# Kernel tuning notes

Measured on AMD Instinct MI355X. Metric: run time of the kernel, lower is better.

## Reference

```python
import jax, jax.numpy as jnp
import numpy as np


def _laplacian(A):
    # D^{-1/2} A D^{-1/2}; original builds diag matrices and does D@A@D,
    # which is mathematically identical to broadcast row/col scaling.
    d = jnp.sum(A, axis=-1)
    dinv = 1.0 / jnp.sqrt(d)
    return A * dinv[:, None] * dinv[None, :]


def _poly(A, theta):
    # P = I + sum_{i=1..k} theta_sig[i-1] * A^i  (theta passed through sigmoid)
    t = jax.nn.sigmoid(theta)
    N = A.shape[-1]
    P = jnp.eye(N, dtype=A.dtype)
    seg = P
    for i in range(theta.shape[0]):  # k is small (2), static loop over poly order
        seg = seg @ A
        P = P + seg * t[i]
    return P


def setup_inputs() -> dict:
    key = jax.random.key(0)
    k1, k2, k3, k4 = jax.random.split(key, 4)
    N, DIN, DOUT, K_CHEB = 4096, 64, 64, 2
    return {
        "x": jax.random.normal(k1, (N, DIN), dtype=jnp.float32),
        "A": jax.random.uniform(k2, (N, N), dtype=jnp.float32),  # positive row sums
        "theta": jax.random.normal(k3, (K_CHEB,), dtype=jnp.float32),
        "W": jax.random.normal(k4, (DOUT, DIN), dtype=jnp.float32) / np.float32(np.sqrt(DIN)),
        "b": jnp.zeros((DOUT,), dtype=jnp.float32),
        "k": 4,
    }


def reference(x, A, theta, W, b, k):
    S = _laplacian(A)
    S = _poly(S, theta)
    S = _laplacian(S)
    # double argsort over last dim = per-row descending rank of each entry
    rank = jnp.argsort(jnp.argsort(-S, axis=-1), axis=-1)
    mask = jnp.where(rank < k, jnp.float32(1.0), jnp.float32(0.0))
    S = S * mask  # keep only top-k entries per row
    x = S @ x     # [N,N] @ [N,DIN]
    return x @ W.T + b  # nn.Linear
```

## Files before the change

### kernel.cpp

```cpp
#include <hip/hip_runtime.h>
#include <hip/hip_bf16.h>
#include <float.h>
#include <math.h>

#define N 4096
#define DIN 64

typedef signed char i8_t;
typedef signed char i8x4 __attribute__((ext_vector_type(4)));
typedef int i32x4 __attribute__((ext_vector_type(4)));
typedef float f32x4 __attribute__((ext_vector_type(4)));

__device__ __forceinline__ void gload16(const void* g, void* l) {
    __builtin_amdgcn_global_load_lds((const __attribute__((address_space(1))) void*)g,
                                     (__attribute__((address_space(3))) void*)l,
                                     16, 0, 0);
}

__device__ __forceinline__ float block_reduce_sum(float s) {
    __shared__ float red[4];
    #pragma unroll
    for (int off = 32; off; off >>= 1) s += __shfl_down(s, off);
    if ((threadIdx.x & 63) == 0) red[threadIdx.x >> 6] = s;
    __syncthreads();
    return red[0] + red[1] + red[2] + red[3];
}

__device__ __forceinline__ bool better(float v1, int j1, float v2, int j2) {
    return v1 > v2 || (v1 == v2 && j1 < j2);
}
__device__ __forceinline__ void ins4(float v, int j, float bv[4], int bj[4]) {
    if (!better(v, j, bv[3], bj[3])) return;
    bv[3] = v; bj[3] = j;
    if (better(bv[3], bj[3], bv[2], bj[2])) {
        float tv = bv[2]; int tj = bj[2]; bv[2] = bv[3]; bj[2] = bj[3]; bv[3] = tv; bj[3] = tj;
    }
    if (better(bv[2], bj[2], bv[1], bj[1])) {
        float tv = bv[1]; int tj = bj[1]; bv[1] = bv[2]; bj[1] = bj[2]; bv[2] = tv; bj[2] = tj;
    }
    if (better(bv[1], bj[1], bv[0], bj[0])) {
        float tv = bv[0]; int tj = bj[0]; bv[0] = bv[1]; bj[0] = bj[1]; bv[1] = tv; bj[1] = tj;
    }
}

__global__ __launch_bounds__(256) void k_rowsum_dinv(const float* __restrict__ A,
                                                     float* __restrict__ dinv,
                                                     float* __restrict__ rowsumP) {
    int row = blockIdx.x, tid = threadIdx.x;
    const float4* a4 = (const float4*)(A + (size_t)row * N);
    float s = 0.f;
    for (int j = tid; j < N / 4; j += 256) {
        float4 v = a4[j];
        s += v.x + v.y + v.z + v.w;
    }
    float tot = block_reduce_sum(s);
    if (tid == 0) {
        dinv[row] = rsqrtf(tot);
        rowsumP[row] = 0.f;
    }
}

__global__ __launch_bounds__(1024) void k_dmax(const float* __restrict__ dinv,
                                               float* __restrict__ dmaxf) {
    int t = threadIdx.x;
    float m = fmaxf(fmaxf(dinv[t], dinv[t + 1024]), fmaxf(dinv[t + 2048], dinv[t + 3072]));
    #pragma unroll
    for (int off = 32; off; off >>= 1) m = fmaxf(m, __shfl_down(m, off));
    __shared__ float red[16];
    if ((t & 63) == 0) red[t >> 6] = m;
    __syncthreads();
    if (t == 0) {
        float mm = red[0];
        #pragma unroll
        for (int i = 1; i < 16; i++) mm = fmaxf(mm, red[i]);
        *dmaxf = mm;
    }
}

__global__ __launch_bounds__(256) void k_make_sqt(const float* __restrict__ A,
                                                  const float* __restrict__ dinv,
                                                  const float* __restrict__ dmaxf,
                                                  i8_t* __restrict__ Sq,
                                                  i8_t* __restrict__ Tq) {
    __shared__ float tile[64][65];
    int tid = threadIdx.x;
    int c4 = tid & 15;
    int rg = tid >> 4;
    int i0 = blockIdx.y * 64;
    int j0 = blockIdx.x * 64;
    float dmax = *dmaxf;
    float sinv = 127.0f / (dmax * dmax);
    float4 dj = *(const float4*)(dinv + j0 + 4 * c4);
    #pragma unroll
    for (int rr = 0; rr < 4; rr++) {
        int r = rg + 16 * rr;
        int row = i0 + r;
        float di = dinv[row];
        float4 av = *(const float4*)(A + (size_t)row * N + j0 + 4 * c4);
        float s0 = av.x * di * dj.x, s1 = av.y * di * dj.y;
        float s2 = av.z * di * dj.z, s3 = av.w * di * dj.w;
        i8x4 qv;
        qv[0] = (i8_t)(int)fminf(rintf(s0 * sinv), 127.f);
        qv[1] = (i8_t)(int)fminf(rintf(s1 * sinv), 127.f);
        qv[2] = (i8_t)(int)fminf(rintf(s2 * sinv), 127.f);
        qv[3] = (i8_t)(int)fminf(rintf(s3 * sinv), 127.f);
        *(i8x4*)(Sq + (size_t)row * N + j0 + 4 * c4) = qv;
        tile[r][4 * c4 + 0] = s0;
        tile[r][4 * c4 + 1] = s1;
        tile[r][4 * c4 + 2] = s2;
        tile[r][4 * c4 + 3] = s3;
    }
    __syncthreads();
    #pragma unroll
    for (int cc = 0; cc < 4; cc++) {
        int c = rg + 16 * cc;
        int gj = j0 + c;
        i8x4 qv;
        #pragma unroll
        for (int u = 0; u < 4; u++)
            qv[u] = (i8_t)(int)fminf(rintf(tile[4 * c4 + u][c] * sinv), 127.f);
        *(i8x4*)(Tq + (size_t)gj * N + i0 + 4 * c4) = qv;
    }
}

__global__ __launch_bounds__(256) void k_xw(const float* __restrict__ x,
                                            const float* __restrict__ W,
                                            float* __restrict__ XW) {
    __shared__ float Wl[64][65];
    __shared__ float xs[4][64];
    int tid = threadIdx.x;
    for (int i = tid; i < 64 * 64; i += 256) Wl[i >> 6][i & 63] = W[i];
    int r = tid >> 6, o = tid & 63;
    int row = blockIdx.x * 4 + r;
    xs[r][o] = x[(size_t)row * DIN + o];
    __syncthreads();
    float acc = 0.f;
    #pragma unroll
    for (int d = 0; d < 64; d++) acc += xs[r][d] * Wl[o][d];
    XW[(size_t)row * DIN + o] = acc;
}

__global__ __launch_bounds__(512, 2) void k_gemm(const i8_t* __restrict__ Sq,
                                                 const i8_t* __restrict__ Tq,
                                                 const float* __restrict__ dmaxf,
                                                 const float* __restrict__ theta,
                                                 float* __restrict__ rowsumP,
                                                 float* __restrict__ candV,
                                                 int* __restrict__ candJ) {
    __shared__ __attribute__((aligned(128))) float pbuf[64][264];
    i8_t* const smem = (i8_t*)pbuf;

    int tid = threadIdx.x;
    int lane = tid & 63;
    int wave = tid >> 6;
    int wr = wave >> 2;
    int wc = wave & 3;

    int bid = blockIdx.x;
    int xcd = bid & 7, local = bid >> 3;
    int bi = ((xcd & 1) << 3) + (local & 7);
    int bj = ((xcd >> 1) << 2) + (local >> 3);

    int qoff = ((tid & 3) ^ ((tid >> 3) & 3)) * 16;
    int row0 = tid >> 2;
    const i8_t* Ag0 = Sq + (size_t)(bi * 256 + row0) * N + qoff;
    const i8_t* Ag1 = Sq + (size_t)(bi * 256 + 128 + row0) * N + qoff;
    const i8_t* Bg0 = Tq + (size_t)(bj * 256 + row0) * N + qoff;
    const i8_t* Bg1 = Tq + (size_t)(bj * 256 + 128 + row0) * N + qoff;
    int l0 = tid * 16;
    int l1 = (tid + 512) * 16;

    i32x4 acc[8][4];
    i32x4 z = {0, 0, 0, 0};
    #pragma unroll
    for (int i = 0; i < 8; i++)
        #pragma unroll
        for (int j = 0; j < 4; j++) acc[i][j] = z;

    int r = lane & 15, q = lane >> 4;
    int qs = q ^ ((r >> 1) & 3);
    int aoff = (wr * 128 + r) * 64 + qs * 16;
    int boff = (wc * 64 + r) * 64 + qs * 16;

    gload16(Ag0, smem + l0);
    gload16(Ag1, smem + l1);
    gload16(Bg0, smem + 16384 + l0);
    gload16(Bg1, smem + 16384 + l1);

    int p = 0;
    for (int t = 0; t < N / 64; ++t) {
        int k1 = (t + 1) * 64;
        if (k1 < N) {
            i8_t* d = smem + (p ^ 1) * 32768;
            gload16(Ag0 + k1, d + l0);
            gload16(Ag1 + k1, d + l1);
            gload16(Bg0 + k1, d + 16384 + l0);
            gload16(Bg1 + k1, d + 16384 + l1);
            asm volatile("s_waitcnt vmcnt(4)" ::: "memory");
        } else {
            asm volatile("s_waitcnt vmcnt(0)" ::: "memory");
        }
        __builtin_amdgcn_s_barrier();

        const i8_t* Ab = smem + p * 32768;
        const i8_t* Bb = Ab + 16384;
        i32x4 af[8], bfr[4];
        #pragma unroll
        for (int mi = 0; mi < 8; mi++) af[mi] = *(const i32x4*)(Ab + aoff + mi * 16 * 64);
        #pragma unroll
        for (int ni = 0; ni < 4; ni++) bfr[ni] = *(const i32x4*)(Bb + boff + ni * 16 * 64);

        __builtin_amdgcn_s_setprio(1);
        #pragma unroll
        for (int mi = 0; mi < 8; mi++)
            #pragma unroll
            for (int ni = 0; ni < 4; ni++)
                acc[mi][ni] = __builtin_amdgcn_mfma_i32_16x16x64_i8(af[mi], bfr[ni],
                                                                    acc[mi][ni], 0, 0, 0);
        __builtin_amdgcn_s_setprio(0);

        asm volatile("s_waitcnt lgkmcnt(0)" ::: "memory");
        __builtin_amdgcn_s_barrier();
        p ^= 1;
    }

    float dmax = *dmaxf;
    float sq = dmax * dmax / 127.0f;
    float t0 = 1.f / (1.f + expf(-theta[0]));
    float t1 = 1.f / (1.f + expf(-theta[1]));
    float t0s = t0 * sq;
    float t1s2 = t1 * sq * sq;
    int col = lane & 15, quad = lane >> 4;

    #pragma unroll
    for (int mi = 0; mi < 8; mi++) {
        int gi0 = bi * 256 + wr * 128 + mi * 16 + quad * 4;
        float rsum[4] = {0.f, 0.f, 0.f, 0.f};
        #pragma unroll
        for (int ni = 0; ni < 4; ni++) {
            int gj = bj * 256 + wc * 64 + ni * 16 + col;
            f32x4 pf;
            #pragma unroll
            for (int rr = 0; rr < 4; rr++) {
                int gi = gi0 + rr;
                float qv = (float)Sq[(size_t)gi * N + gj];
                float p2 = t1s2 * (float)acc[mi][ni][rr] + t0s * qv + ((gi == gj) ? 1.f : 0.f);
                pf[rr] = p2;
                rsum[rr] += p2;
            }
            acc[mi][ni] = __builtin_bit_cast(i32x4, pf);
        }
        #pragma unroll
        for (int rr = 0; rr < 4; rr++) {
            float v = rsum[rr];
            v += __shfl_xor(v, 1);
            v += __shfl_xor(v, 2);
            v += __shfl_xor(v, 4);
            v += __shfl_xor(v, 8);
            if (col == 0) atomicAdd(&rowsumP[gi0 + rr], v);
        }
    }

    int srow = tid >> 3;
    int sub = tid & 7;
    __syncthreads();

    #pragma unroll
    for (int pass = 0; pass < 4; pass++) {
        if (wr == (pass >> 1)) {
            int mi0 = (pass & 1) * 4;
            #pragma unroll
            for (int m2 = 0; m2 < 4; m2++) {
                #pragma unroll
                for (int ni = 0; ni < 4; ni++) {
                    f32x4 pf = __builtin_bit_cast(f32x4, acc[mi0 + m2][ni]);
                    #pragma unroll
                    for (int rr = 0; rr < 4; rr++)
                        pbuf[m2 * 16 + quad * 4 + rr][wc * 64 + ni * 16 + col] = pf[rr];
                }
            }
        }
        __syncthreads();
        float bv[4] = {-FLT_MAX, -FLT_MAX, -FLT_MAX, -FLT_MAX};
        int bjx[4] = {N, N, N, N};
        int jbase = bj * 256;
        for (int i = 0; i < 32; i++) {
            int c = i * 8 + sub;
            ins4(pbuf[srow][c], jbase + c, bv, bjx);
        }
        #pragma unroll
        for (int off = 1; off < 8; off <<= 1) {
            float ov[4]; int oj[4];
            #pragma unroll
            for (int c = 0; c < 4; c++) { ov[c] = __shfl_xor(bv[c], off); oj[c] = __shfl_xor(bjx[c], off); }
            #pragma unroll
            for (int c = 0; c < 4; c++) ins4(ov[c], oj[c], bv, bjx);
        }
        if (sub == 0) {
            size_t base = ((size_t)(bi * 256 + pass * 64 + srow) * 16 + bj) * 4;
            #pragma unroll
            for (int c = 0; c < 4; c++) { candV[base + c] = bv[c]; candJ[base + c] = bjx[c]; }
        }
        __syncthreads();
    }
}

__global__ __launch_bounds__(256) void k_dinv2(const float* __restrict__ rowsumP,
                                               float* __restrict__ dinv2) {
    int g = blockIdx.x * 256 + threadIdx.x;
    dinv2[g] = rsqrtf(rowsumP[g]);
}

__global__ __launch_bounds__(64) void k_final(const float* __restrict__ candV,
                                              const int* __restrict__ candJ,
                                              const float* __restrict__ dinv2,
                                              const float* __restrict__ XW,
                                              const float* __restrict__ bvec,
                                              const int* __restrict__ kin,
                                              float* __restrict__ out) {
    int row = blockIdx.x, t = threadIdx.x;
    float cv = candV[(size_t)row * 64 + t];
    int cj = candJ[(size_t)row * 64 + t];
    float bv[4] = {-FLT_MAX, -FLT_MAX, -FLT_MAX, -FLT_MAX};
    int bj[4] = {N, N, N, N};
    ins4(cv * dinv2[cj], cj, bv, bj);
    #pragma unroll
    for (int off = 1; off < 64; off <<= 1) {
        float ov[4]; int oj[4];
        #pragma unroll
        for (int c = 0; c < 4; c++) { ov[c] = __shfl_xor(bv[c], off); oj[c] = __shfl_xor(bj[c], off); }
        #pragma unroll
        for (int c = 0; c < 4; c++) ins4(ov[c], oj[c], bv, bj);
    }
    int kk = kin[0];
    if (kk > 4) kk = 4;
    if (kk < 0) kk = 0;
    float sc = dinv2[row];
    float o = bvec[t];
    for (int c = 0; c < kk; c++)
        o += sc * bv[c] * XW[(size_t)bj[c] * DIN + t];
    out[(size_t)row * DIN + t] = o;
}

extern "C" void kernel_launch(void* const* d_in, const int* in_sizes, int n_in,
                              void* d_out, int out_size, void* d_ws, size_t ws_size,
                              hipStream_t stream) {
    const float* x = (const float*)d_in[0];
    const float* A = (const float*)d_in[1];
    const float* theta = (const float*)d_in[2];
    const float* W = (const float*)d_in[3];
    const float* b = (const float*)d_in[4];
    const int* kin = (const int*)d_in[5];
    float* out = (float*)d_out;

    char* ws = (char*)d_ws;
    i8_t* Sq = (i8_t*)ws;
    i8_t* Tq = (i8_t*)(ws + (size_t)N * N);
    float* candV = (float*)(ws + (size_t)N * N * 2);
    int* candJ = (int*)(ws + (size_t)N * N * 2 + (size_t)N * 64 * 4);
    float* dinv = (float*)(ws + (size_t)N * N * 2 + (size_t)N * 64 * 8);
    float* dinv2 = dinv + N;
    float* rowsumP = dinv2 + N;
    float* dmaxf = rowsumP + N;
    float* XW = (float*)(ws + (size_t)N * N * 2 + (size_t)N * 64 * 8 + 65536);

    k_xw<<<N / 4, 256, 0, stream>>>(x, W, XW);
    k_rowsum_dinv<<<N, 256, 0, stream>>>(A, dinv, rowsumP);
    k_dmax<<<1, 1024, 0, stream>>>(dinv, dmaxf);
    k_make_sqt<<<dim3(64, 64), 256, 0, stream>>>(A, dinv, dmaxf, Sq, Tq);
    k_gemm<<<256, 512, 0, stream>>>(Sq, Tq, dmaxf, theta, rowsumP, candV, candJ);
    k_dinv2<<<N / 256, 256, 0, stream>>>(rowsumP, dinv2);
    k_final<<<N, 64, 0, stream>>>(candV, candJ, dinv2, XW, b, kin, out);
}
```

Measured before the change: 261.6 us.

## Triple-buffer int8 GEMM LDS tiles and interleave loads with MFMA phases

Moves the int8 MFMA GEMM main loop from double to triple buffering in LDS, prefetching two k-tiles ahead. Each iteration is split into four phases. Every phase loads two A fragments, issues one of the four global-to-LDS prefetch loads, and runs eight MFMAs, all separated by barriers and sched_barrier. The aim is to hide global load latency and spread LDS traffic across the MFMA work. The cost is more LDS per block (96KB), which may reduce occupancy below the launch bound of 2 blocks, plus many extra barriers per iteration.

```diff
diff --git a/kernel.cpp b/kernel.cpp
--- a/kernel.cpp
+++ b/kernel.cpp
@@ -147,8 +147,8 @@
                                                  float* __restrict__ rowsumP,
                                                  float* __restrict__ candV,
                                                  int* __restrict__ candJ) {
-    __shared__ __attribute__((aligned(128))) float pbuf[64][264];
-    i8_t* const smem = (i8_t*)pbuf;
+    __shared__ __attribute__((aligned(128))) i8_t smem[3 * 32768];
+    float (*pbuf)[264] = (float (*)[264])smem;
 
     int tid = threadIdx.x;
     int lane = tid & 63;
@@ -186,43 +186,65 @@
     gload16(Ag1, smem + l1);
     gload16(Bg0, smem + 16384 + l0);
     gload16(Bg1, smem + 16384 + l1);
-
-    int p = 0;
-    for (int t = 0; t < N / 64; ++t) {
-        int k1 = (t + 1) * 64;
-        if (k1 < N) {
-            i8_t* d = smem + (p ^ 1) * 32768;
-            gload16(Ag0 + k1, d + l0);
-            gload16(Ag1 + k1, d + l1);
-            gload16(Bg0 + k1, d + 16384 + l0);
-            gload16(Bg1 + k1, d + 16384 + l1);
-            asm volatile("s_waitcnt vmcnt(4)" ::: "memory");
-        } else {
-            asm volatile("s_waitcnt vmcnt(0)" ::: "memory");
-        }
+    gload16(Ag0 + 64, smem + 32768 + l0);
+    gload16(Ag1 + 64, smem + 32768 + l1);
+    gload16(Bg0 + 64, smem + 32768 + 16384 + l0);
+    gload16(Bg1 + 64, smem + 32768 + 16384 + l1);
+
+#define MFMA_ROW(af_, mi_)                                                            \
+    acc[mi_][0] = __builtin_amdgcn_mfma_i32_16x16x64_i8(af_, b0, acc[mi_][0], 0, 0, 0); \
+    acc[mi_][1] = __builtin_amdgcn_mfma_i32_16x16x64_i8(af_, b1, acc[mi_][1], 0, 0, 0); \
+    acc[mi_][2] = __builtin_amdgcn_mfma_i32_16x16x64_i8(af_, b2, acc[mi_][2], 0, 0, 0); \
+    acc[mi_][3] = __builtin_amdgcn_mfma_i32_16x16x64_i8(af_, b3, acc[mi_][3], 0, 0, 0);
+
+    int pb = 0;
+    for (int t = 0; t < 64; ++t) {
+        const i8_t* Ab = smem + pb * 32768;
+        const i8_t* Bb = Ab + 16384;
+        int pb2 = pb + 2; if (pb2 >= 3) pb2 -= 3;
+        i8_t* d = smem + pb2 * 32768;
+        int k2 = (t + 2) * 64;
+        bool pf = (t < 62);
+
+        if (t < 63) { asm volatile("s_waitcnt vmcnt(4)" ::: "memory"); }
+        else        { asm volatile("s_waitcnt vmcnt(0)" ::: "memory"); }
         __builtin_amdgcn_s_barrier();
-
-        const i8_t* Ab = smem + p * 32768;
-        const i8_t* Bb = Ab + 16384;
-        i32x4 af[8], bfr[4];
-        #pragma unroll
-        for (int mi = 0; mi < 8; mi++) af[mi] = *(const i32x4*)(Ab + aoff + mi * 16 * 64);
-        #pragma unroll
-        for (int ni = 0; ni < 4; ni++) bfr[ni] = *(const i32x4*)(Bb + boff + ni * 16 * 64);
-
+        i32x4 a0 = *(const i32x4*)(Ab + aoff);
+        i32x4 a1 = *(const i32x4*)(Ab + aoff + 1024);
+        i32x4 b0 = *(const i32x4*)(Bb + boff);
+        i32x4 b1 = *(const i32x4*)(Bb + boff + 1024);
+        i32x4 b2 = *(const i32x4*)(Bb + boff + 2048);
+        i32x4 b3 = *(const i32x4*)(Bb + boff + 3072);
+        if (pf) gload16(Ag0 + k2, d + l0);
+        asm volatile("s_waitcnt lgkmcnt(0)" ::: "memory");
+        __builtin_amdgcn_sched_barrier(0);
         __builtin_amdgcn_s_setprio(1);
-        #pragma unroll
-        for (int mi = 0; mi < 8; mi++)
-            #pragma unroll
-            for (int ni = 0; ni < 4; ni++)
-                acc[mi][ni] = __builtin_amdgcn_mfma_i32_16x16x64_i8(af[mi], bfr[ni],
-                                                                    acc[mi][ni], 0, 0, 0);
+        MFMA_ROW(a0, 0)
+        MFMA_ROW(a1, 1)
         __builtin_amdgcn_s_setprio(0);
-
-        asm volatile("s_waitcnt lgkmcnt(0)" ::: "memory");
         __builtin_amdgcn_s_barrier();
-        p ^= 1;
-    }
+
+        #pragma unroll
+        for (int ph = 1; ph < 4; ++ph) {
+            i32x4 aa0 = *(const i32x4*)(Ab + aoff + (2 * ph) * 1024);
+            i32x4 aa1 = *(const i32x4*)(Ab + aoff + (2 * ph + 1) * 1024);
+            if (pf) {
+                if (ph == 1) gload16(Ag1 + k2, d + l1);
+                if (ph == 2) gload16(Bg0 + k2, d + 16384 + l0);
+                if (ph == 3) gload16(Bg1 + k2, d + 16384 + l1);
+            }
+            __builtin_amdgcn_s_barrier();
+            asm volatile("s_waitcnt lgkmcnt(0)" ::: "memory");
+            __builtin_amdgcn_sched_barrier(0);
+            __builtin_amdgcn_s_setprio(1);
+            MFMA_ROW(aa0, 2 * ph)
+            MFMA_ROW(aa1, 2 * ph + 1)
+            __builtin_amdgcn_s_setprio(0);
+            __builtin_amdgcn_s_barrier();
+        }
+        pb++; if (pb == 3) pb = 0;
+    }
+#undef MFMA_ROW
 
     float dmax = *dmaxf;
     float sq = dmax * dmax / 127.0f;
```

After: 252.0 us. -3.6%, faster.

## Fuse small prep kernels, stage Sq tile in LDS for epilogue, drop dinv2 kernel

Applied to the files above, without the earlier changes.

Merges the XW projection, row-sum and dmax into one launch, with dmax computed through an atomicMax on float bits after a memset. This removes the separate dmax and dinv2 kernels. The GEMM epilogue now reads the int8 S tile through a swizzled async global-to-LDS load instead of scattered byte loads from global memory. k_final packs four rows per block and computes rsqrt inline. The intent is to cut launch overhead and uncoalesced epilogue reads, at the cost of an extra LDS fill and a barrier after the main loop.

```diff
diff --git a/kernel.cpp b/kernel.cpp
--- a/kernel.cpp
+++ b/kernel.cpp
@@ -43,10 +43,30 @@
     }
 }
 
-__global__ __launch_bounds__(256) void k_rowsum_dinv(const float* __restrict__ A,
-                                                     float* __restrict__ dinv,
-                                                     float* __restrict__ rowsumP) {
-    int row = blockIdx.x, tid = threadIdx.x;
+__global__ __launch_bounds__(256) void k_pre(const float* __restrict__ A,
+                                             const float* __restrict__ x,
+                                             const float* __restrict__ W,
+                                             float* __restrict__ dinv,
+                                             float* __restrict__ rowsumP,
+                                             float* __restrict__ dmaxf,
+                                             float* __restrict__ XW) {
+    int tid = threadIdx.x;
+    if (blockIdx.x >= N) {
+        __shared__ float Wl[64][65];
+        __shared__ float xs[4][64];
+        int bx = blockIdx.x - N;
+        for (int i = tid; i < 64 * 64; i += 256) Wl[i >> 6][i & 63] = W[i];
+        int r = tid >> 6, o = tid & 63;
+        int row = bx * 4 + r;
+        xs[r][o] = x[(size_t)row * DIN + o];
+        __syncthreads();
+        float acc = 0.f;
+        #pragma unroll
+        for (int d = 0; d < 64; d++) acc += xs[r][d] * Wl[o][d];
+        XW[(size_t)row * DIN + o] = acc;
+        return;
+    }
+    int row = blockIdx.x;
     const float4* a4 = (const float4*)(A + (size_t)row * N);
     float s = 0.f;
     for (int j = tid; j < N / 4; j += 256) {
@@ -55,25 +75,10 @@
     }
     float tot = block_reduce_sum(s);
     if (tid == 0) {
-        dinv[row] = rsqrtf(tot);
+        float v = rsqrtf(tot);
+        dinv[row] = v;
         rowsumP[row] = 0.f;
-    }
-}
-
-__global__ __launch_bounds__(1024) void k_dmax(const float* __restrict__ dinv,
-                                               float* __restrict__ dmaxf) {
-    int t = threadIdx.x;
-    float m = fmaxf(fmaxf(dinv[t], dinv[t + 1024]), fmaxf(dinv[t + 2048], dinv[t + 3072]));
-    #pragma unroll
-    for (int off = 32; off; off >>= 1) m = fmaxf(m, __shfl_down(m, off));
-    __shared__ float red[16];
-    if ((t & 63) == 0) red[t >> 6] = m;
-    __syncthreads();
-    if (t == 0) {
-        float mm = red[0];
-        #pragma unroll
-        for (int i = 1; i < 16; i++) mm = fmaxf(mm, red[i]);
-        *dmaxf = mm;
+        atomicMax((unsigned int*)dmaxf, __float_as_uint(v));
     }
 }
 
@@ -123,23 +128,6 @@
     }
 }
 
-__global__ __launch_bounds__(256) void k_xw(const float* __restrict__ x,
-                                            const float* __restrict__ W,
-                                            float* __restrict__ XW) {
-    __shared__ float Wl[64][65];
-    __shared__ float xs[4][64];
-    int tid = threadIdx.x;
-    for (int i = tid; i < 64 * 64; i += 256) Wl[i >> 6][i & 63] = W[i];
-    int r = tid >> 6, o = tid & 63;
-    int row = blockIdx.x * 4 + r;
-    xs[r][o] = x[(size_t)row * DIN + o];
-    __syncthreads();
-    float acc = 0.f;
-    #pragma unroll
-    for (int d = 0; d < 64; d++) acc += xs[r][d] * Wl[o][d];
-    XW[(size_t)row * DIN + o] = acc;
-}
-
 __global__ __launch_bounds__(512, 2) void k_gemm(const i8_t* __restrict__ Sq,
                                                  const i8_t* __restrict__ Tq,
                                                  const float* __restrict__ dmaxf,
@@ -147,8 +135,8 @@
                                                  float* __restrict__ rowsumP,
                                                  float* __restrict__ candV,
                                                  int* __restrict__ candJ) {
-    __shared__ __attribute__((aligned(128))) float pbuf[64][264];
-    i8_t* const smem = (i8_t*)pbuf;
+    __shared__ __attribute__((aligned(128))) i8_t smem[67584];
+    float (*pbuf)[264] = (float (*)[264])smem;
 
     int tid = threadIdx.x;
     int lane = tid & 63;
@@ -224,6 +212,17 @@
         p ^= 1;
     }
 
+    #pragma unroll
+    for (int u = 0; u < 8; u++) {
+        int o = (u * 512 + tid) * 16;
+        int rrow = o >> 8;
+        int ch = (o >> 4) & 15;
+        int sch = ch ^ ((rrow >> 2) & 3);
+        gload16(Sq + (size_t)(bi * 256 + rrow) * N + bj * 256 + sch * 16, smem + o);
+    }
+    asm volatile("s_waitcnt vmcnt(0)" ::: "memory");
+    __syncthreads();
+
     float dmax = *dmaxf;
     float sq = dmax * dmax / 127.0f;
     float t0 = 1.f / (1.f + expf(-theta[0]));
@@ -234,17 +233,21 @@
 
     #pragma unroll
     for (int mi = 0; mi < 8; mi++) {
-        int gi0 = bi * 256 + wr * 128 + mi * 16 + quad * 4;
+        int lrow0 = wr * 128 + mi * 16 + quad * 4;
+        int gi0 = bi * 256 + lrow0;
         float rsum[4] = {0.f, 0.f, 0.f, 0.f};
         #pragma unroll
         for (int ni = 0; ni < 4; ni++) {
-            int gj = bj * 256 + wc * 64 + ni * 16 + col;
+            int colb = wc * 64 + ni * 16 + col;
+            int gj = bj * 256 + colb;
             f32x4 pf;
             #pragma unroll
             for (int rr = 0; rr < 4; rr++) {
-                int gi = gi0 + rr;
-                float qv = (float)Sq[(size_t)gi * N + gj];
-                float p2 = t1s2 * (float)acc[mi][ni][rr] + t0s * qv + ((gi == gj) ? 1.f : 0.f);
+                int lrow = lrow0 + rr;
+                int ch = (colb >> 4) ^ ((lrow >> 2) & 3);
+                float qv = (float)smem[lrow * 256 + ch * 16 + col];
+                float p2 = t1s2 * (float)acc[mi][ni][rr] + t0s * qv
+                           + ((gi0 + rr == gj) ? 1.f : 0.f);
                 pf[rr] = p2;
                 rsum[rr] += p2;
             }
@@ -305,25 +308,21 @@
     }
 }
 
-__global__ __launch_bounds__(256) void k_dinv2(const float* __restrict__ rowsumP,
-                                               float* __restrict__ dinv2) {
-    int g = blockIdx.x * 256 + threadIdx.x;
-    dinv2[g] = rsqrtf(rowsumP[g]);
-}
-
-__global__ __launch_bounds__(64) void k_final(const float* __restrict__ candV,
-                                              const int* __restrict__ candJ,
-                                              const float* __restrict__ dinv2,
-                                              const float* __restrict__ XW,
-                                              const float* __restrict__ bvec,
-                                              const int* __restrict__ kin,
-                                              float* __restrict__ out) {
-    int row = blockIdx.x, t = threadIdx.x;
+__global__ __launch_bounds__(256) void k_final(const float* __restrict__ candV,
+                                               const int* __restrict__ candJ,
+                                               const float* __restrict__ rowsumP,
+                                               const float* __restrict__ XW,
+                                               const float* __restrict__ bvec,
+                                               const int* __restrict__ kin,
+                                               float* __restrict__ out) {
+    int tid = threadIdx.x;
+    int row = blockIdx.x * 4 + (tid >> 6);
+    int t = tid & 63;
     float cv = candV[(size_t)row * 64 + t];
     int cj = candJ[(size_t)row * 64 + t];
     float bv[4] = {-FLT_MAX, -FLT_MAX, -FLT_MAX, -FLT_MAX};
     int bj[4] = {N, N, N, N};
-    ins4(cv * dinv2[cj], cj, bv, bj);
+    ins4(cv * rsqrtf(rowsumP[cj]), cj, bv, bj);
     #pragma unroll
     for (int off = 1; off < 64; off <<= 1) {
         float ov[4]; int oj[4];
@@ -335,7 +334,7 @@
     int kk = kin[0];
     if (kk > 4) kk = 4;
     if (kk < 0) kk = 0;
-    float sc = dinv2[row];
+    float sc = rsqrtf(rowsumP[row]);
     float o = bvec[t];
     for (int c = 0; c < kk; c++)
         o += sc * bv[c] * XW[(size_t)bj[c] * DIN + t];
@@ -359,16 +358,13 @@
     float* candV = (float*)(ws + (size_t)N * N * 2);
     int* candJ = (int*)(ws + (size_t)N * N * 2 + (size_t)N * 64 * 4);
     float* dinv = (float*)(ws + (size_t)N * N * 2 + (size_t)N * 64 * 8);
-    float* dinv2 = dinv + N;
-    float* rowsumP = dinv2 + N;
+    float* rowsumP = dinv + N;
     float* dmaxf = rowsumP + N;
     float* XW = (float*)(ws + (size_t)N * N * 2 + (size_t)N * 64 * 8 + 65536);
 
-    k_xw<<<N / 4, 256, 0, stream>>>(x, W, XW);
-    k_rowsum_dinv<<<N, 256, 0, stream>>>(A, dinv, rowsumP);
-    k_dmax<<<1, 1024, 0, stream>>>(dinv, dmaxf);
+    hipMemsetAsync(dmaxf, 0, 4, stream);
+    k_pre<<<N + N / 4, 256, 0, stream>>>(A, x, W, dinv, rowsumP, dmaxf, XW);
     k_make_sqt<<<dim3(64, 64), 256, 0, stream>>>(A, dinv, dmaxf, Sq, Tq);
     k_gemm<<<256, 512, 0, stream>>>(Sq, Tq, dmaxf, theta, rowsumP, candV, candJ);
-    k_dinv2<<<N / 256, 256, 0, stream>>>(rowsumP, dinv2);
-    k_final<<<N, 64, 0, stream>>>(candV, candJ, dinv2, XW, b, kin, out);
-}
+    k_final<<<N / 4, 256, 0, stream>>>(candV, candJ, rowsumP, XW, b, kin, out);
+}
```

Measured after the change: 290.7 us. 11.1% more time.

## Deepen int8 GEMM pipeline to four LDS stages and stage epilogue tile in LDS

Applied to the files above, without the earlier changes.

Moves the int8 MFMA GEMM main loop from double to quad buffering in LDS, keeping three tiles of global loads in flight and issuing each prefetch after the barrier. The goal is to hide global memory latency better. The epilogue now bulk-loads the 256x256 int8 Sq tile into LDS with a swizzle through async global-to-LDS loads, replacing scattered per-element global byte reads. LDS use grows to 128KB per block, which may reduce occupancy below the launch bound of 2 blocks per CU.

```diff
diff --git a/kernel.cpp b/kernel.cpp
--- a/kernel.cpp
+++ b/kernel.cpp
@@ -147,8 +147,8 @@
                                                  float* __restrict__ rowsumP,
                                                  float* __restrict__ candV,
                                                  int* __restrict__ candJ) {
-    __shared__ __attribute__((aligned(128))) float pbuf[64][264];
-    i8_t* const smem = (i8_t*)pbuf;
+    __shared__ __attribute__((aligned(128))) i8_t smem[4 * 32768];
+    float (*pbuf)[264] = (float (*)[264])smem;
 
     int tid = threadIdx.x;
     int lane = tid & 63;
@@ -182,27 +182,31 @@
     int aoff = (wr * 128 + r) * 64 + qs * 16;
     int boff = (wc * 64 + r) * 64 + qs * 16;
 
-    gload16(Ag0, smem + l0);
-    gload16(Ag1, smem + l1);
-    gload16(Bg0, smem + 16384 + l0);
-    gload16(Bg1, smem + 16384 + l1);
-
-    int p = 0;
+    #pragma unroll
+    for (int pt = 0; pt < 3; ++pt) {
+        i8_t* d = smem + pt * 32768;
+        gload16(Ag0 + pt * 64, d + l0);
+        gload16(Ag1 + pt * 64, d + l1);
+        gload16(Bg0 + pt * 64, d + 16384 + l0);
+        gload16(Bg1 + pt * 64, d + 16384 + l1);
+    }
+
     for (int t = 0; t < N / 64; ++t) {
-        int k1 = (t + 1) * 64;
-        if (k1 < N) {
-            i8_t* d = smem + (p ^ 1) * 32768;
-            gload16(Ag0 + k1, d + l0);
-            gload16(Ag1 + k1, d + l1);
-            gload16(Bg0 + k1, d + 16384 + l0);
-            gload16(Bg1 + k1, d + 16384 + l1);
-            asm volatile("s_waitcnt vmcnt(4)" ::: "memory");
-        } else {
-            asm volatile("s_waitcnt vmcnt(0)" ::: "memory");
-        }
+        if (t <= 61)      { asm volatile("s_waitcnt vmcnt(8)" ::: "memory"); }
+        else if (t == 62) { asm volatile("s_waitcnt vmcnt(4)" ::: "memory"); }
+        else              { asm volatile("s_waitcnt vmcnt(0)" ::: "memory"); }
         __builtin_amdgcn_s_barrier();
 
-        const i8_t* Ab = smem + p * 32768;
+        if (t + 3 < N / 64) {
+            i8_t* d = smem + ((t + 3) & 3) * 32768;
+            int k3 = (t + 3) * 64;
+            gload16(Ag0 + k3, d + l0);
+            gload16(Ag1 + k3, d + l1);
+            gload16(Bg0 + k3, d + 16384 + l0);
+            gload16(Bg1 + k3, d + 16384 + l1);
+        }
+
+        const i8_t* Ab = smem + (t & 3) * 32768;
         const i8_t* Bb = Ab + 16384;
         i32x4 af[8], bfr[4];
         #pragma unroll
@@ -221,8 +225,18 @@
 
         asm volatile("s_waitcnt lgkmcnt(0)" ::: "memory");
         __builtin_amdgcn_s_barrier();
-        p ^= 1;
-    }
+    }
+
+    #pragma unroll
+    for (int u = 0; u < 8; u++) {
+        int o = (u * 512 + tid) * 16;
+        int rrow = o >> 8;
+        int ch = (o >> 4) & 15;
+        int sch = ch ^ ((rrow >> 2) & 3);
+        gload16(Sq + (size_t)(bi * 256 + rrow) * N + bj * 256 + sch * 16, smem + o);
+    }
+    asm volatile("s_waitcnt vmcnt(0)" ::: "memory");
+    __syncthreads();
 
     float dmax = *dmaxf;
     float sq = dmax * dmax / 127.0f;
@@ -234,17 +248,21 @@
 
     #pragma unroll
     for (int mi = 0; mi < 8; mi++) {
-        int gi0 = bi * 256 + wr * 128 + mi * 16 + quad * 4;
+        int lrow0 = wr * 128 + mi * 16 + quad * 4;
+        int gi0 = bi * 256 + lrow0;
         float rsum[4] = {0.f, 0.f, 0.f, 0.f};
         #pragma unroll
         for (int ni = 0; ni < 4; ni++) {
-            int gj = bj * 256 + wc * 64 + ni * 16 + col;
+            int colb = wc * 64 + ni * 16 + col;
+            int gj = bj * 256 + colb;
             f32x4 pf;
             #pragma unroll
             for (int rr = 0; rr < 4; rr++) {
-                int gi = gi0 + rr;
-                float qv = (float)Sq[(size_t)gi * N + gj];
-                float p2 = t1s2 * (float)acc[mi][ni][rr] + t0s * qv + ((gi == gj) ? 1.f : 0.f);
+                int lrow = lrow0 + rr;
+                int ch = ((colb >> 4) ^ ((lrow >> 2) & 3));
+                float qv = (float)smem[lrow * 256 + ch * 16 + col];
+                float p2 = t1s2 * (float)acc[mi][ni][rr] + t0s * qv
+                           + ((gi0 + rr == gj) ? 1.f : 0.f);
                 pf[rr] = p2;
                 rsum[rr] += p2;
             }
```

Result: no change. 256.7 us, median of 3 (-1.9%).
